# Performance work log

Measured on AMD Instinct MI355X. Metric: run time of the kernel, lower is better.

## Reference

```python
import jax, jax.numpy as jnp
import numpy as np

NUM_HEADS = 16

def setup_inputs() -> dict:
    key = jax.random.key(0)
    ks = jax.random.split(key, 7)
    n_node, n_graph, E = 512, 8, 1024
    H = NUM_HEADS
    inp = {
        "query": jax.random.normal(ks[0], (n_node, n_graph, E), jnp.float32),
        "attn_bias": jax.random.normal(ks[1], (n_graph * H, n_node, n_node), jnp.float32),
        "graph_attn_weight": jax.random.normal(ks[2], (n_graph * H, n_node, n_node), jnp.float32),
        "in_w": jax.random.normal(ks[3], (3 * E, E), jnp.float32) * (E ** -0.5),
        "in_b": jnp.zeros((3 * E,), jnp.float32),
        "out_w": jax.random.normal(ks[4], (E, E), jnp.float32) * (E ** -0.5),
        "out_b": jnp.zeros((E,), jnp.float32),
    }
    return inp

def reference(query, attn_bias, graph_attn_weight, in_w, in_b, out_w, out_b):
    n_node, n_graph, E = query.shape
    H = NUM_HEADS
    hd = E // H
    scaling = hd ** -0.5
    # fused QKV projection (torch Linear: x @ W.T + b)
    qkv = query @ in_w.T + in_b                      # [n, g, 3E]
    q, k, v = jnp.split(qkv, 3, axis=-1)             # each [n, g, E]
    def to_heads(x):
        # [n, g, E] -> [g*H, n, hd]
        return x.reshape(n_node, n_graph * H, hd).transpose(1, 0, 2)
    q = to_heads(q) * scaling
    k = to_heads(k)
    v = to_heads(v)
    attn_weights = jnp.einsum('bnd,bmd->bnm', q, k) + attn_bias  # [g*H, n, n]
    attn_probs = jnp.tanh(graph_attn_weight) * jax.nn.softmax(attn_weights, axis=-1)
    attn = jnp.einsum('bnm,bmd->bnd', attn_probs, v)             # [g*H, n, hd]
    attn = attn.transpose(1, 0, 2).reshape(n_node, n_graph, E)
    return attn @ out_w.T + out_b
```

## Files before the change

kernel.cpp:

```cpp
#include <hip/hip_runtime.h>
#include <hip/hip_bf16.h>
#include <cstdint>

#define N_NODE 512
#define N_GRAPH 8
#define EDIM 1024
#define NHEADS 16
#define HD 64
#define GH 128
#define MROWS 4096

typedef short bf16x8 __attribute__((ext_vector_type(8)));
typedef float f32x4  __attribute__((ext_vector_type(4)));

__device__ __forceinline__ short f2bs(float f) {
    union { __hip_bfloat16 h; short s; } u; u.h = __float2bfloat16(f); return u.s;
}
__device__ __forceinline__ float bs2f(short s) {
    union { unsigned u; float f; } v; v.u = ((unsigned)(unsigned short)s) << 16; return v.f;
}
__device__ __forceinline__ float fast_tanh(float x) {
    const float e = __expf(2.f * x);
    return 1.f - __fdividef(2.f, 1.f + e);
}

__device__ __forceinline__ void direct_lds16(const short* g, short* l) {
    __builtin_amdgcn_global_load_lds(
        (const __attribute__((address_space(1))) unsigned int*)(uintptr_t)g,
        (__attribute__((address_space(3))) unsigned int*)(unsigned)(uintptr_t)l,
        16, 0, 0);
}

__global__ __launch_bounds__(256)
void cvt_bf16(const float* __restrict__ in, short* __restrict__ out, int n8)
{
    const int i = blockIdx.x * 256 + threadIdx.x;
    if (i >= n8) return;
    const float4 f0 = *reinterpret_cast<const float4*>(in + (size_t)i * 8);
    const float4 f1 = *reinterpret_cast<const float4*>(in + (size_t)i * 8 + 4);
    bf16x8 h;
    h[0] = f2bs(f0.x); h[1] = f2bs(f0.y); h[2] = f2bs(f0.z); h[3] = f2bs(f0.w);
    h[4] = f2bs(f1.x); h[5] = f2bs(f1.y); h[6] = f2bs(f1.z); h[7] = f2bs(f1.w);
    *reinterpret_cast<bf16x8*>(out + (size_t)i * 8) = h;
}

template<int MODE>
__global__ __launch_bounds__(256)
void gemm_bf16(const short* __restrict__ A, const short* __restrict__ B,
               const float* __restrict__ bias, float* __restrict__ Cout,
               __hip_bfloat16* __restrict__ Cq,
               __hip_bfloat16* __restrict__ Ck,
               __hip_bfloat16* __restrict__ Cv,
               int M, int N, int K)
{
    __shared__ short As[128 * 32];
    __shared__ short Bs[128 * 32];

    const int tid  = threadIdx.x;
    const int m0   = blockIdx.y * 128;
    const int n0   = blockIdx.x * 128;
    const int lane = tid & 63;
    const int w    = tid >> 6;
    const int l16  = lane & 15;
    const int quad = lane >> 4;
    const int wm   = w & 1;
    const int wn   = w >> 1;
    const int lrow = lane >> 2;
    const int lcol = (lane & 3) << 3;

    const short* ga = A + (size_t)(m0 + w * 16 + lrow) * K + lcol;
    const short* gb = B + (size_t)(n0 + w * 16 + lrow) * K + lcol;
    short* lA = &As[w * 512];
    short* lB = &Bs[w * 512];

    f32x4 acc[4][4];
    #pragma unroll
    for (int mt = 0; mt < 4; mt++)
        #pragma unroll
        for (int nt = 0; nt < 4; nt++)
            acc[mt][nt] = (f32x4){0.f, 0.f, 0.f, 0.f};

    for (int k0 = 0; k0 < K; k0 += 32) {
        direct_lds16(ga + k0, lA);
        direct_lds16(ga + (size_t)64 * K + k0, lA + 2048);
        direct_lds16(gb + k0, lB);
        direct_lds16(gb + (size_t)64 * K + k0, lB + 2048);
        __syncthreads();

        bf16x8 af[4], bfr[4];
        #pragma unroll
        for (int mt = 0; mt < 4; mt++)
            af[mt] = *reinterpret_cast<const bf16x8*>(
                &As[(wm * 64 + mt * 16 + l16) * 32 + quad * 8]);
        #pragma unroll
        for (int nt = 0; nt < 4; nt++)
            bfr[nt] = *reinterpret_cast<const bf16x8*>(
                &Bs[(wn * 64 + nt * 16 + l16) * 32 + quad * 8]);
        #pragma unroll
        for (int mt = 0; mt < 4; mt++)
            #pragma unroll
            for (int nt = 0; nt < 4; nt++)
                acc[mt][nt] = __builtin_amdgcn_mfma_f32_16x16x32_bf16(
                    af[mt], bfr[nt], acc[mt][nt], 0, 0, 0);
        __syncthreads();
    }

    #pragma unroll
    for (int nt = 0; nt < 4; nt++) {
        const int c = n0 + wn * 64 + nt * 16 + l16;
        const float bv = bias[c];
        #pragma unroll
        for (int mt = 0; mt < 4; mt++) {
            #pragma unroll
            for (int rr = 0; rr < 4; rr++) {
                const int r = m0 + wm * 64 + mt * 16 + quad * 4 + rr;
                const float v = acc[mt][nt][rr] + bv;
                if (MODE == 0) {
                    Cout[(size_t)r * N + c] = v;
                } else {
                    const int qsel = c >> 10;
                    const int e = c & 1023;
                    const int head = e >> 6;
                    const int d = e & 63;
                    const int node = r >> 3;
                    const int graph = r & 7;
                    const int b = graph * NHEADS + head;
                    const size_t idx = ((size_t)b * N_NODE + node) * HD + d;
                    if (qsel == 0)      Cq[idx] = __float2bfloat16(v * 0.125f);
                    else if (qsel == 1) Ck[idx] = __float2bfloat16(v);
                    else                Cv[idx] = __float2bfloat16(v);
                }
            }
        }
    }
}

__global__ __launch_bounds__(256)
void transpose_v(const __hip_bfloat16* __restrict__ V,
                 __hip_bfloat16* __restrict__ Vt)
{
    __shared__ short T[64][80];
    const int b = blockIdx.y;
    const int jt = blockIdx.x;
    const int t = threadIdx.x;

    #pragma unroll
    for (int it = 0; it < 2; it++) {
        const int idx = t + it * 256;
        const int j_loc = idx >> 3;
        const int ch = idx & 7;
        bf16x8 v = *reinterpret_cast<const bf16x8*>(
            V + ((size_t)b * N_NODE + jt * 64 + j_loc) * HD + ch * 8);
        *reinterpret_cast<bf16x8*>(&T[j_loc][ch * 8]) = v;
    }
    __syncthreads();
    #pragma unroll
    for (int it = 0; it < 2; it++) {
        const int idx = t + it * 256;
        const int d_loc = idx >> 3;
        const int ch = idx & 7;
        bf16x8 o;
        #pragma unroll
        for (int x = 0; x < 8; x++) o[x] = T[ch * 8 + x][d_loc];
        *reinterpret_cast<bf16x8*>(
            Vt + ((size_t)b * HD + d_loc) * N_NODE + jt * 64 + ch * 8) = o;
    }
}

#define SSF 517
#define SPB 520

__global__ __launch_bounds__(256)
void attn_mfma(const __hip_bfloat16* __restrict__ Qh,
               const __hip_bfloat16* __restrict__ Kh,
               const __hip_bfloat16* __restrict__ Vt,
               const float* __restrict__ bias,
               const float* __restrict__ gaw,
               __hip_bfloat16* __restrict__ A2)
{
    __shared__ __align__(16) float S[16][SSF];
    __shared__ __align__(16) short Pb[16][SPB];
    __shared__ __align__(16) float mpart[16][4];
    __shared__ float rrs[16];

    const int b    = blockIdx.y;
    const int i0   = blockIdx.x * 16;
    const int tid  = threadIdx.x;
    const int lane = tid & 63;
    const int w    = tid >> 6;
    const int quad = lane >> 4;
    const int l16  = lane & 15;

    {
        const __hip_bfloat16* Qb =
            Qh + ((size_t)b * N_NODE + i0 + l16) * HD + quad * 8;
        const bf16x8 qa0 = *reinterpret_cast<const bf16x8*>(Qb);
        const bf16x8 qa1 = *reinterpret_cast<const bf16x8*>(Qb + 32);
        const int row_l = quad * 4;
        const float* bp0 = bias + ((size_t)b * N_NODE + i0 + row_l) * N_NODE + l16;
        float mxr[4] = {-1e30f, -1e30f, -1e30f, -1e30f};

        #pragma unroll 2
        for (int jt = w; jt < 32; jt += 4) {
            const __hip_bfloat16* Kb =
                Kh + ((size_t)b * N_NODE + jt * 16 + l16) * HD + quad * 8;
            const bf16x8 k0 = *reinterpret_cast<const bf16x8*>(Kb);
            const bf16x8 k1 = *reinterpret_cast<const bf16x8*>(Kb + 32);
            f32x4 acc = {0.f, 0.f, 0.f, 0.f};
            acc = __builtin_amdgcn_mfma_f32_16x16x32_bf16(qa0, k0, acc, 0, 0, 0);
            acc = __builtin_amdgcn_mfma_f32_16x16x32_bf16(qa1, k1, acc, 0, 0, 0);
            const float* bp = bp0 + jt * 16;
            #pragma unroll
            for (int r = 0; r < 4; r++) {
                const float v = acc[r] + bp[(size_t)r * N_NODE];
                S[row_l + r][jt * 16 + l16] = v;
                mxr[r] = fmaxf(mxr[r], v);
            }
        }
        #pragma unroll
        for (int r = 0; r < 4; r++) {
            float m = mxr[r];
            m = fmaxf(m, __shfl_xor(m, 1));
            m = fmaxf(m, __shfl_xor(m, 2));
            m = fmaxf(m, __shfl_xor(m, 4));
            m = fmaxf(m, __shfl_xor(m, 8));
            if (l16 == 0) mpart[row_l + r][w] = m;
        }
    }
    __syncthreads();

    {
        const int r   = tid >> 4;
        const int c16 = tid & 15;
        const float4 mp = *reinterpret_cast<const float4*>(mpart[r]);
        const float m = fmaxf(fmaxf(mp.x, mp.y), fmaxf(mp.z, mp.w));
        float sum = 0.f;
        #pragma unroll 4
        for (int jj = 0; jj < 32; jj++) {
            const float e = __expf(S[r][c16 + 16 * jj] - m);
            sum += e;
            Pb[r][c16 + 16 * jj] = f2bs(e);
        }
        sum += __shfl_xor(sum, 1);
        sum += __shfl_xor(sum, 2);
        sum += __shfl_xor(sum, 4);
        sum += __shfl_xor(sum, 8);
        if (c16 == 0) rrs[r] = 1.f / sum;
    }
    __syncthreads();

    {
        const float* gb = gaw + ((size_t)b * N_NODE + i0) * N_NODE;
        #pragma unroll 2
        for (int it = 0; it < 8; it++) {
            const int idx = tid * 4 + it * 1024;
            const int r = idx >> 9;
            const int j = idx & 511;
            const float4 g = *reinterpret_cast<const float4*>(gb + idx);
            const short4 e4 = *reinterpret_cast<const short4*>(&Pb[r][j]);
            short4 o4;
            o4.x = f2bs(fast_tanh(g.x) * bs2f(e4.x));
            o4.y = f2bs(fast_tanh(g.y) * bs2f(e4.y));
            o4.z = f2bs(fast_tanh(g.z) * bs2f(e4.z));
            o4.w = f2bs(fast_tanh(g.w) * bs2f(e4.w));
            *reinterpret_cast<short4*>(&Pb[r][j]) = o4;
        }
    }
    __syncthreads();

    {
        const __hip_bfloat16* Vb =
            Vt + ((size_t)b * HD + w * 16 + l16) * N_NODE + quad * 8;
        f32x4 acc = {0.f, 0.f, 0.f, 0.f};
        #pragma unroll 4
        for (int j32 = 0; j32 < 16; j32++) {
            const bf16x8 af =
                *reinterpret_cast<const bf16x8*>(&Pb[l16][j32 * 32 + quad * 8]);
            const bf16x8 bfr = *reinterpret_cast<const bf16x8*>(Vb + j32 * 32);
            acc = __builtin_amdgcn_mfma_f32_16x16x32_bf16(af, bfr, acc, 0, 0, 0);
        }
        const int node0 = i0 + quad * 4;
        __hip_bfloat16* op = A2 + (size_t)node0 * (N_GRAPH * EDIM)
                           + (b >> 4) * EDIM + (b & 15) * HD + w * 16 + l16;
        #pragma unroll
        for (int r = 0; r < 4; r++)
            op[(size_t)r * (N_GRAPH * EDIM)] =
                __float2bfloat16(acc[r] * rrs[quad * 4 + r]);
    }
}

extern "C" void kernel_launch(void* const* d_in, const int* in_sizes, int n_in,
                              void* d_out, int out_size, void* d_ws, size_t ws_size,
                              hipStream_t stream) {
    const float* query     = (const float*)d_in[0];
    const float* attn_bias = (const float*)d_in[1];
    const float* gaw       = (const float*)d_in[2];
    const float* in_w      = (const float*)d_in[3];
    const float* in_b      = (const float*)d_in[4];
    const float* out_w     = (const float*)d_in[5];
    const float* out_b     = (const float*)d_in[6];
    float* out = (float*)d_out;

    short* wsp = (short*)d_ws;
    const size_t hsz = (size_t)GH * N_NODE * HD;
    short* Q   = wsp;
    short* K   = wsp + hsz;
    short* V   = wsp + 2 * hsz;
    short* Vt  = wsp + 3 * hsz;
    short* A2  = V;
    short* qb  = Vt;
    short* wbi = wsp + 4 * hsz;
    short* wbo = wbi + (size_t)3 * EDIM * EDIM;

    cvt_bf16<<<dim3(MROWS * EDIM / 2048), 256, 0, stream>>>(query, qb, MROWS * EDIM / 8);
    cvt_bf16<<<dim3(3 * EDIM * EDIM / 2048), 256, 0, stream>>>(in_w, wbi, 3 * EDIM * EDIM / 8);
    cvt_bf16<<<dim3(EDIM * EDIM / 2048), 256, 0, stream>>>(out_w, wbo, EDIM * EDIM / 8);

    gemm_bf16<1><<<dim3(24, 32), 256, 0, stream>>>(
        qb, wbi, in_b, nullptr,
        (__hip_bfloat16*)Q, (__hip_bfloat16*)K, (__hip_bfloat16*)V,
        MROWS, 3 * EDIM, EDIM);

    transpose_v<<<dim3(8, GH), 256, 0, stream>>>(
        (const __hip_bfloat16*)V, (__hip_bfloat16*)Vt);

    attn_mfma<<<dim3(N_NODE / 16, GH), 256, 0, stream>>>(
        (const __hip_bfloat16*)Q, (const __hip_bfloat16*)K,
        (const __hip_bfloat16*)Vt, attn_bias, gaw, (__hip_bfloat16*)A2);

    gemm_bf16<0><<<dim3(8, 32), 256, 0, stream>>>(
        (const short*)A2, wbo, out_b, out,
        nullptr, nullptr, nullptr, MROWS, EDIM, EDIM);
}
```

Measured before the change: 434.4 us.

## Keep attention scores in registers, fuse softmax with tanh gating, swizzle LDS

The attention kernel now keeps the QK^T+bias scores in registers instead of staging them in a 16x517 float shared buffer. The exp, the row sum and the tanh(gaw) multiply are fused into a single pass that writes bf16 probabilities into an XOR-swizzled 16x512 LDS buffer, which removes one barrier and one LDS round trip. Row sums become per-wave partials that are combined at the output, and the launch bounds now ask for 4 blocks per CU. The GEMM kernel also remaps its block indices with a stride-8 swizzle to change how tiles are spread across XCDs and caches. The register-resident scores may add register pressure, and the gaw loads change from float4 to scalar strided loads.

```diff
diff --git a/kernel.cpp b/kernel.cpp
--- a/kernel.cpp
+++ b/kernel.cpp
@@ -56,9 +56,16 @@
     __shared__ short As[128 * 32];
     __shared__ short Bs[128 * 32];
 
+    const int nwg  = gridDim.x * gridDim.y;
+    const int flat = blockIdx.y * gridDim.x + blockIdx.x;
+    const int q8   = nwg >> 3;
+    const int swz  = (flat & 7) * q8 + (flat >> 3);
+    const int bx   = swz % gridDim.x;
+    const int by   = swz / gridDim.x;
+
     const int tid  = threadIdx.x;
-    const int m0   = blockIdx.y * 128;
-    const int n0   = blockIdx.x * 128;
+    const int m0   = by * 128;
+    const int n0   = bx * 128;
     const int lane = tid & 63;
     const int w    = tid >> 6;
     const int l16  = lane & 15;
@@ -167,10 +174,9 @@
     }
 }
 
-#define SSF 517
-#define SPB 520
-
-__global__ __launch_bounds__(256)
+#define PBS 512
+
+__global__ __launch_bounds__(256, 4)
 void attn_mfma(const __hip_bfloat16* __restrict__ Qh,
                const __hip_bfloat16* __restrict__ Kh,
                const __hip_bfloat16* __restrict__ Vt,
@@ -178,10 +184,9 @@
                const float* __restrict__ gaw,
                __hip_bfloat16* __restrict__ A2)
 {
-    __shared__ __align__(16) float S[16][SSF];
-    __shared__ __align__(16) short Pb[16][SPB];
+    __shared__ __align__(16) short Pb[16 * PBS];
     __shared__ __align__(16) float mpart[16][4];
-    __shared__ float rrs[16];
+    __shared__ __align__(16) float spart[16][4];
 
     const int b    = blockIdx.y;
     const int i0   = blockIdx.x * 16;
@@ -190,18 +195,21 @@
     const int w    = tid >> 6;
     const int quad = lane >> 4;
     const int l16  = lane & 15;
+    const int row_l = quad * 4;
+
+    f32x4 sreg[8];
 
     {
         const __hip_bfloat16* Qb =
             Qh + ((size_t)b * N_NODE + i0 + l16) * HD + quad * 8;
         const bf16x8 qa0 = *reinterpret_cast<const bf16x8*>(Qb);
         const bf16x8 qa1 = *reinterpret_cast<const bf16x8*>(Qb + 32);
-        const int row_l = quad * 4;
         const float* bp0 = bias + ((size_t)b * N_NODE + i0 + row_l) * N_NODE + l16;
-        float mxr[4] = {-1e30f, -1e30f, -1e30f, -1e30f};
-
-        #pragma unroll 2
-        for (int jt = w; jt < 32; jt += 4) {
+        float mx[4] = {-1e30f, -1e30f, -1e30f, -1e30f};
+
+        #pragma unroll
+        for (int t = 0; t < 8; t++) {
+            const int jt = w + 4 * t;
             const __hip_bfloat16* Kb =
                 Kh + ((size_t)b * N_NODE + jt * 16 + l16) * HD + quad * 8;
             const bf16x8 k0 = *reinterpret_cast<const bf16x8*>(Kb);
@@ -212,14 +220,14 @@
             const float* bp = bp0 + jt * 16;
             #pragma unroll
             for (int r = 0; r < 4; r++) {
-                const float v = acc[r] + bp[(size_t)r * N_NODE];
-                S[row_l + r][jt * 16 + l16] = v;
-                mxr[r] = fmaxf(mxr[r], v);
+                acc[r] += bp[(size_t)r * N_NODE];
+                mx[r] = fmaxf(mx[r], acc[r]);
             }
+            sreg[t] = acc;
         }
         #pragma unroll
         for (int r = 0; r < 4; r++) {
-            float m = mxr[r];
+            float m = mx[r];
             m = fmaxf(m, __shfl_xor(m, 1));
             m = fmaxf(m, __shfl_xor(m, 2));
             m = fmaxf(m, __shfl_xor(m, 4));
@@ -230,40 +238,39 @@
     __syncthreads();
 
     {
-        const int r   = tid >> 4;
-        const int c16 = tid & 15;
-        const float4 mp = *reinterpret_cast<const float4*>(mpart[r]);
-        const float m = fmaxf(fmaxf(mp.x, mp.y), fmaxf(mp.z, mp.w));
-        float sum = 0.f;
-        #pragma unroll 4
-        for (int jj = 0; jj < 32; jj++) {
-            const float e = __expf(S[r][c16 + 16 * jj] - m);
-            sum += e;
-            Pb[r][c16 + 16 * jj] = f2bs(e);
-        }
-        sum += __shfl_xor(sum, 1);
-        sum += __shfl_xor(sum, 2);
-        sum += __shfl_xor(sum, 4);
-        sum += __shfl_xor(sum, 8);
-        if (c16 == 0) rrs[r] = 1.f / sum;
-    }
-    __syncthreads();
-
-    {
-        const float* gb = gaw + ((size_t)b * N_NODE + i0) * N_NODE;
-        #pragma unroll 2
-        for (int it = 0; it < 8; it++) {
-            const int idx = tid * 4 + it * 1024;
-            const int r = idx >> 9;
-            const int j = idx & 511;
-            const float4 g = *reinterpret_cast<const float4*>(gb + idx);
-            const short4 e4 = *reinterpret_cast<const short4*>(&Pb[r][j]);
-            short4 o4;
-            o4.x = f2bs(fast_tanh(g.x) * bs2f(e4.x));
-            o4.y = f2bs(fast_tanh(g.y) * bs2f(e4.y));
-            o4.z = f2bs(fast_tanh(g.z) * bs2f(e4.z));
-            o4.w = f2bs(fast_tanh(g.w) * bs2f(e4.w));
-            *reinterpret_cast<short4*>(&Pb[r][j]) = o4;
+        float mrow[4];
+        #pragma unroll
+        for (int r = 0; r < 4; r++) {
+            const float4 mp = *reinterpret_cast<const float4*>(mpart[row_l + r]);
+            mrow[r] = fmaxf(fmaxf(mp.x, mp.y), fmaxf(mp.z, mp.w));
+        }
+        float sum[4] = {0.f, 0.f, 0.f, 0.f};
+        const float* gp0 = gaw + ((size_t)b * N_NODE + i0 + row_l) * N_NODE + l16;
+
+        #pragma unroll
+        for (int t = 0; t < 8; t++) {
+            const int jt = w + 4 * t;
+            const int colb = (jt * 16 + l16) * 2;
+            const float* gp = gp0 + jt * 16;
+            #pragma unroll
+            for (int r = 0; r < 4; r++) {
+                const float e = __expf(sreg[t][r] - mrow[r]);
+                sum[r] += e;
+                const float g = gp[(size_t)r * N_NODE];
+                const float p = fast_tanh(g) * e;
+                const int row = row_l + r;
+                const int byte = row * (PBS * 2) + (colb ^ ((row & 7) << 4));
+                *reinterpret_cast<short*>(reinterpret_cast<char*>(Pb) + byte) = f2bs(p);
+            }
+        }
+        #pragma unroll
+        for (int r = 0; r < 4; r++) {
+            float s = sum[r];
+            s += __shfl_xor(s, 1);
+            s += __shfl_xor(s, 2);
+            s += __shfl_xor(s, 4);
+            s += __shfl_xor(s, 8);
+            if (l16 == 0) spart[row_l + r][w] = s;
         }
     }
     __syncthreads();
@@ -272,10 +279,12 @@
         const __hip_bfloat16* Vb =
             Vt + ((size_t)b * HD + w * 16 + l16) * N_NODE + quad * 8;
         f32x4 acc = {0.f, 0.f, 0.f, 0.f};
-        #pragma unroll 4
+        #pragma unroll
         for (int j32 = 0; j32 < 16; j32++) {
-            const bf16x8 af =
-                *reinterpret_cast<const bf16x8*>(&Pb[l16][j32 * 32 + quad * 8]);
+            const int byte = l16 * (PBS * 2)
+                           + ((j32 * 64 + quad * 16) ^ ((l16 & 7) << 4));
+            const bf16x8 af = *reinterpret_cast<const bf16x8*>(
+                reinterpret_cast<const char*>(Pb) + byte);
             const bf16x8 bfr = *reinterpret_cast<const bf16x8*>(Vb + j32 * 32);
             acc = __builtin_amdgcn_mfma_f32_16x16x32_bf16(af, bfr, acc, 0, 0, 0);
         }
@@ -283,9 +292,11 @@
         __hip_bfloat16* op = A2 + (size_t)node0 * (N_GRAPH * EDIM)
                            + (b >> 4) * EDIM + (b & 15) * HD + w * 16 + l16;
         #pragma unroll
-        for (int r = 0; r < 4; r++)
-            op[(size_t)r * (N_GRAPH * EDIM)] =
-                __float2bfloat16(acc[r] * rrs[quad * 4 + r]);
+        for (int r = 0; r < 4; r++) {
+            const float4 sp = *reinterpret_cast<const float4*>(spart[quad * 4 + r]);
+            const float rs = 1.f / (sp.x + sp.y + sp.z + sp.w);
+            op[(size_t)r * (N_GRAPH * EDIM)] = __float2bfloat16(acc[r] * rs);
+        }
     }
 }
 
```

New measurement: 426.7 us. Within noise of the previous version (-1.8%).
